# Kernel tuning notes

Hardware: AMD Instinct MI355X
Metric: run time of the kernel (lower is better)

The kernel has to match this reference:

```python
import jax, jax.numpy as jnp
import numpy as np

B, MAXN, D, H, S = 64, 512, 512, 8, 32
DH = D // H          # per-head dim = 64
N = B * MAXN         # 32768 total nodes
E = 524288           # ~avg degree 16
EPS = 1e-5


def setup_inputs() -> dict:
    key = jax.random.key(0)
    ks = jax.random.split(key, 18)
    s = 0.05
    x_dense = jax.random.normal(ks[0], (B, MAXN, D), jnp.float32)
    x = jax.random.normal(ks[1], (N, D), jnp.float32)
    src = jax.random.randint(ks[2], (E,), 0, N)
    # destinations kept within the same graph as the source
    dst = (src // MAXN) * MAXN + jax.random.randint(ks[3], (E,), 0, MAXN)
    edge_index = jnp.stack([src, dst]).astype(jnp.int32)
    batch = (jnp.arange(N) // MAXN).astype(jnp.int32)  # sorted, 512 nodes/graph
    seed = jax.random.normal(ks[4], (S, 1, D), jnp.float32) * s
    # per-head GCN conv weights concatenated along output dim: [D, H*DH] == [D, D]
    Wk = jax.random.normal(ks[5], (D, D), jnp.float32) * s
    bk = jnp.zeros((D,), jnp.float32)
    Wv = jax.random.normal(ks[6], (D, D), jnp.float32) * s
    bv = jnp.zeros((D,), jnp.float32)
    q_proj_weight = jax.random.normal(ks[7], (D, D), jnp.float32) * s
    Wo = jax.random.normal(ks[8], (D, D), jnp.float32) * s
    bo = jnp.zeros((D,), jnp.float32)
    Wff = jax.random.normal(ks[9], (D, D), jnp.float32) * s
    bff = jnp.zeros((D,), jnp.float32)
    gamma_h = jnp.ones((D,), jnp.float32)
    beta_h = jnp.zeros((D,), jnp.float32)
    gamma_z = jnp.ones((D,), jnp.float32)
    beta_z = jnp.zeros((D,), jnp.float32)
    return dict(x_dense=x_dense, x=x, edge_index=edge_index, batch=batch,
                seed=seed, Wk=Wk, bk=bk, Wv=Wv, bv=bv,
                q_proj_weight=q_proj_weight, Wo=Wo, bo=bo, Wff=Wff, bff=bff,
                gamma_h=gamma_h, beta_h=beta_h, gamma_z=gamma_z, beta_z=beta_z)


def _gcn(x, W, b, src, dst):
    # PyG GCNConv with self-loops + symmetric norm; all H heads fused via W [D, H*DH]
    xw = x @ W                                   # [N, D]
    idx = jnp.arange(N)
    src_f = jnp.concatenate([src, idx])
    dst_f = jnp.concatenate([dst, idx])
    deg = jax.ops.segment_sum(jnp.ones_like(dst_f, dtype=x.dtype), dst_f, num_segments=N)
    dinv = jax.lax.rsqrt(deg)                    # deg >= 1 (self-loops)
    norm = dinv[src_f] * dinv[dst_f]             # [E+N]
    out = jax.ops.segment_sum(xw[src_f] * norm[:, None], dst_f, num_segments=N)
    return out + b


def _to_dense(feat, batch):
    # to_dense_batch for sorted batch vector; padded slots are zeros
    counts = jax.ops.segment_sum(jnp.ones((N,), jnp.int32), batch, num_segments=B)
    start = jnp.cumsum(counts) - counts
    pos = jnp.arange(N) - start[batch]
    return jnp.zeros((B, MAXN, feat.shape[-1]), feat.dtype).at[batch, pos].set(feat)


def _layernorm(x, g, b):
    m = jnp.mean(x, -1, keepdims=True)
    v = jnp.mean(jnp.square(x - m), -1, keepdims=True)
    return (x - m) * jax.lax.rsqrt(v + EPS) * g + b


def reference(x_dense, x, edge_index, batch, seed, Wk, bk, Wv, bv,
              q_proj_weight, Wo, bo, Wff, bff, gamma_h, beta_h, gamma_z, beta_z):
    src, dst = edge_index[0], edge_index[1]
    k_nodes = _gcn(x, Wk, bk, src, dst)          # [N, D] (H heads concat)
    v_nodes = _gcn(x, Wv, bv, src, dst)
    k_dense = _to_dense(k_nodes, batch)          # [B, MAXN, D]
    v_dense = _to_dense(v_nodes, batch)

    # query: seed [S,1,D] repeated over batch -> [S,B,D]; q projection (F.linear)
    query = jnp.broadcast_to(seed, (S, B, D))
    q = jnp.einsum('sbd,ed->sbe', query, q_proj_weight)
    scale = 1.0 / jnp.sqrt(jnp.float32(DH))
    qh = (q * scale).reshape(S, B, H, DH).transpose(1, 2, 0, 3)     # [B,H,S,DH]
    kh = k_dense.reshape(B, MAXN, H, DH).transpose(0, 2, 1, 3)      # [B,H,N,DH]
    vh = v_dense.reshape(B, MAXN, H, DH).transpose(0, 2, 1, 3)
    scores = jnp.einsum('bhsd,bhnd->bhsn', qh, kh)                  # [B,H,S,MAXN]
    attn = jax.nn.softmax(scores, axis=-1)                          # no padding mask (faithful)
    ctx = jnp.einsum('bhsn,bhnd->bhsd', attn, vh)                   # [B,H,S,DH]
    ctx = ctx.transpose(0, 2, 1, 3).reshape(B, S, D)                # heads concat
    attn_out = ctx @ Wo.T + bo                                      # [B,S,D]

    query_bse = jnp.broadcast_to(seed.transpose(1, 0, 2), (B, S, D))
    embed = _layernorm(query_bse + attn_out, gamma_h, beta_h)
    embed = _layernorm(embed + embed @ Wff.T + bff, gamma_z, beta_z)
    return embed
```

## Files before the change

kernel.cpp:

```cpp
#include <hip/hip_runtime.h>
#include <hip/hip_bf16.h>

#define BN   64
#define MAXN 512
#define DIM  512
#define NH   8
#define NS   32
#define DHD  64
#define NN   32768
#define NE   524288

typedef __hip_bfloat16 bf16;
using bf16x8 = __attribute__((ext_vector_type(8))) short;
using f32x4  = __attribute__((ext_vector_type(4))) float;

__device__ int   g_cnt[NN];
__device__ int   g_cur[NN];
__device__ int   g_off[NN + 1];
__device__ int   g_csr[NE];
__device__ float g_dinv[NN];
__device__ bf16  g_xb[NN * DIM];
__device__ bf16  g_agg[NN * DIM];
__device__ bf16  g_kv[NN * 2 * DIM];
__device__ bf16  g_wkvT[2 * DIM * DIM];
__device__ bf16  g_woT[DIM * DIM];
__device__ bf16  g_wffT[DIM * DIM];
__device__ float g_biaskv[2 * DIM];
__device__ float g_q[NS * DIM];
__device__ bf16  g_qb[NS * DIM];
__device__ bf16  g_ctx[BN * NS * DIM];
__device__ float g_tmp[BN * NS * DIM];
__device__ float g_h1[BN * NS * DIM];
__device__ bf16  g_h1b[BN * NS * DIM];

__device__ inline float bf2f(unsigned short u) {
    union { unsigned int i; float f; } x; x.i = ((unsigned int)u) << 16; return x.f;
}

__device__ inline void gll16(const bf16* g, bf16* l) {
    __builtin_amdgcn_global_load_lds(
        (const __attribute__((address_space(1))) void*)g,
        (__attribute__((address_space(3))) void*)l, 16, 0, 0);
}

__global__ void k_zero() {
    int i = blockIdx.x * 256 + threadIdx.x;
    if (i < NN) { g_cnt[i] = 0; g_cur[i] = 0; }
}

__global__ void k_count(const int* __restrict__ dst) {
    int e = blockIdx.x * 256 + threadIdx.x;
    if (e < NE) atomicAdd(&g_cnt[dst[e]], 1);
}

__global__ void k_scan() {
    __shared__ int part[1024];
    int t = threadIdx.x;
    int base = t * 32;
    int loc[32]; int s = 0;
#pragma unroll
    for (int i = 0; i < 32; i++) { loc[i] = g_cnt[base + i]; s += loc[i]; }
    part[t] = s; __syncthreads();
    for (int o = 1; o < 1024; o <<= 1) {
        int v = (t >= o) ? part[t - o] : 0;
        __syncthreads();
        part[t] += v;
        __syncthreads();
    }
    int ex = (t == 0) ? 0 : part[t - 1];
#pragma unroll
    for (int i = 0; i < 32; i++) { g_off[base + i] = ex; ex += loc[i]; }
    if (t == 1023) g_off[NN] = ex;
}

__global__ void k_dinv() {
    int i = blockIdx.x * 256 + threadIdx.x;
    if (i < NN) g_dinv[i] = rsqrtf(1.0f + (float)g_cnt[i]);
}

__global__ void k_fill(const int* __restrict__ src, const int* __restrict__ dst) {
    int e = blockIdx.x * 256 + threadIdx.x;
    if (e < NE) {
        int d = dst[e];
        int p = atomicAdd(&g_cur[d], 1);
        g_csr[g_off[d] + p] = src[e];
    }
}

__global__ __launch_bounds__(256) void k_xb(const float* __restrict__ x) {
    long i = (long)(blockIdx.x * 256 + threadIdx.x) * 8;
    int node = (int)(i >> 9);
    float w = g_dinv[node];
    float4 a = *(const float4*)(x + i);
    float4 b = *(const float4*)(x + i + 4);
    float v[8] = {a.x, a.y, a.z, a.w, b.x, b.y, b.z, b.w};
    bf16x8 o;
#pragma unroll
    for (int j = 0; j < 8; j++) { bf16 t = __float2bfloat16(v[j] * w); o[j] = *(short*)&t; }
    *(bf16x8*)(g_xb + i) = o;
}

__global__ __launch_bounds__(256) void k_gather() {
    int bid = blockIdx.x;
    int lb = (bid & 7) * 1024 + (bid >> 3);
    int wave = threadIdx.x >> 6, lane = threadIdx.x & 63;
    int node = lb * 4 + wave;

    bf16x8 sv = ((const bf16x8*)(g_xb + (long)node * DIM))[lane];
    float acc[8];
#pragma unroll
    for (int j = 0; j < 8; j++) acc[j] = bf2f((unsigned short)sv[j]);

    int e = g_off[node], e1 = g_off[node + 1];
    for (; e + 2 <= e1; e += 2) {
        int s0 = g_csr[e], s1 = g_csr[e + 1];
        bf16x8 r0 = ((const bf16x8*)(g_xb + (long)s0 * DIM))[lane];
        bf16x8 r1 = ((const bf16x8*)(g_xb + (long)s1 * DIM))[lane];
#pragma unroll
        for (int j = 0; j < 8; j++)
            acc[j] += bf2f((unsigned short)r0[j]) + bf2f((unsigned short)r1[j]);
    }
    if (e < e1) {
        int s0 = g_csr[e];
        bf16x8 r0 = ((const bf16x8*)(g_xb + (long)s0 * DIM))[lane];
#pragma unroll
        for (int j = 0; j < 8; j++) acc[j] += bf2f((unsigned short)r0[j]);
    }
    float dd = g_dinv[node];
    bf16x8 o;
#pragma unroll
    for (int j = 0; j < 8; j++) { bf16 t = __float2bfloat16(acc[j] * dd); o[j] = *(short*)&t; }
    ((bf16x8*)(g_agg + (long)node * DIM))[lane] = o;
}

__global__ void k_prepw(const float* __restrict__ Wk, const float* __restrict__ Wv,
                        const float* __restrict__ bk, const float* __restrict__ bv,
                        const float* __restrict__ Wo, const float* __restrict__ Wff) {
    int i = blockIdx.x * 256 + threadIdx.x;
    int c = i >> 9, k = i & 511;
    float v = (c < DIM) ? Wk[k * DIM + c] : Wv[k * DIM + (c - DIM)];
    g_wkvT[i] = __float2bfloat16(v);
    if (i < DIM * DIM) {
        g_woT[i]  = __float2bfloat16(Wo[i]);
        g_wffT[i] = __float2bfloat16(Wff[i]);
    }
    if (i < 2 * DIM) g_biaskv[i] = (i < DIM) ? bk[i] : bv[i - DIM];
}

__global__ void k_qproj(const float* __restrict__ seed, const float* __restrict__ Wq) {
    int i = blockIdx.x * 256 + threadIdx.x;
    int s = i >> 9, e = i & 511;
    const float* sr = seed + s * DIM;
    const float* wr = Wq + e * DIM;
    float acc = 0.f;
    for (int d = 0; d < DIM; d += 4) {
        float4 a = *(const float4*)(sr + d);
        float4 b = *(const float4*)(wr + d);
        acc += a.x * b.x + a.y * b.y + a.z * b.z + a.w * b.w;
    }
    float qv = acc * 0.125f;
    g_q[i] = qv;
    g_qb[i] = __float2bfloat16(qv);
}

template<int W>
__global__ __launch_bounds__(256) void k_gemm(const float* __restrict__ biasIn) {
    constexpr int Nout = (W == 0) ? 2 * DIM : DIM;
    const bf16* A  = (W == 0) ? g_agg  : (W == 1) ? g_ctx : g_h1b;
    const bf16* Bt = (W == 0) ? g_wkvT : (W == 1) ? g_woT : g_wffT;
    const float* bias = (W == 0) ? g_biaskv : biasIn;

    __shared__ bf16 As[2][128 * 32];
    __shared__ bf16 Bs[2][128 * 32];
    int tid = threadIdx.x;
    int lane = tid & 63, wave = tid >> 6;
    int wr = wave >> 1, wc = wave & 1;
    long row0 = (long)blockIdx.x * 128, col0 = (long)blockIdx.y * 128;
    f32x4 acc[4][4];
#pragma unroll
    for (int i = 0; i < 4; i++)
#pragma unroll
        for (int j = 0; j < 4; j++) acc[i][j] = (f32x4){0.f, 0.f, 0.f, 0.f};
    int fr = lane & 15, fq = lane >> 4;
    int sw = (fr >> 1) & 3;
    int rchunk = (fq ^ sw) * 8;

    int u0 = wave * 128 + lane;
    int s_row[2], s_col[2];
#pragma unroll
    for (int c = 0; c < 2; c++) {
        int u = u0 + c * 64;
        int row = u >> 2, cc = u & 3;
        s_row[c] = row;
        s_col[c] = (cc ^ ((row >> 1) & 3)) * 8;
    }

    auto stage = [&](int buf, int kt) {
#pragma unroll
        for (int c = 0; c < 2; c++)
            gll16(A + (row0 + s_row[c]) * DIM + kt + s_col[c], As[buf] + (u0 + c * 64) * 8);
#pragma unroll
        for (int c = 0; c < 2; c++)
            gll16(Bt + (col0 + s_row[c]) * DIM + kt + s_col[c], Bs[buf] + (u0 + c * 64) * 8);
    };

    stage(0, 0);
    __syncthreads();

    for (int kt = 0; kt < DIM; kt += 32) {
        int buf = (kt >> 5) & 1;
        if (kt + 32 < DIM) stage(buf ^ 1, kt + 32);
        bf16x8 af[4], bfv[4];
#pragma unroll
        for (int mi = 0; mi < 4; mi++)
            af[mi] = *(const bf16x8*)(As[buf] + (wr * 64 + mi * 16 + fr) * 32 + rchunk);
#pragma unroll
        for (int ni = 0; ni < 4; ni++)
            bfv[ni] = *(const bf16x8*)(Bs[buf] + (wc * 64 + ni * 16 + fr) * 32 + rchunk);
#pragma unroll
        for (int mi = 0; mi < 4; mi++)
#pragma unroll
            for (int ni = 0; ni < 4; ni++)
                acc[mi][ni] = __builtin_amdgcn_mfma_f32_16x16x32_bf16(af[mi], bfv[ni], acc[mi][ni], 0, 0, 0);
        __syncthreads();
    }
#pragma unroll
    for (int mi = 0; mi < 4; mi++)
#pragma unroll
        for (int ni = 0; ni < 4; ni++) {
            long col = col0 + wc * 64 + ni * 16 + fr;
            float bv = bias[col];
#pragma unroll
            for (int r = 0; r < 4; r++) {
                long row = row0 + wr * 64 + mi * 16 + fq * 4 + r;
                float v = acc[mi][ni][r] + bv;
                if constexpr (W == 0) g_kv[row * Nout + col] = __float2bfloat16(v);
                else                  g_tmp[row * Nout + col] = v;
            }
        }
}

__global__ __launch_bounds__(512) void k_attn() {
    __shared__ bf16  kv[64 * 72];
    __shared__ float sc[32 * 516];
    __shared__ float rs[NS];
    int b = blockIdx.x >> 3, h = blockIdx.x & 7;
    int tid = threadIdx.x;
    int lane = tid & 63, w = tid >> 6;
    int fr = lane & 15, fq = lane >> 4;
    int stile = w >> 2;
    int nsub  = w & 3;
    int dht   = w & 3;

    const unsigned short* KV = (const unsigned short*)g_kv + (long)b * MAXN * (2 * DIM) + h * DHD;
    int srow = tid >> 3;
    int scol = (tid & 7) * 8;

    bf16x8 qf[2];
#pragma unroll
    for (int k0 = 0; k0 < 2; k0++)
        qf[k0] = *(const bf16x8*)(g_qb + (long)(stile * 16 + fr) * DIM + h * DHD + k0 * 32 + fq * 8);

    int4 pre = *(const int4*)(KV + (long)srow * (2 * DIM) + scol);
    for (int t = 0; t < 8; t++) {
        __syncthreads();
        *(int4*)((unsigned short*)kv + srow * 72 + scol) = pre;
        if (t < 7) pre = *(const int4*)(KV + (long)((t + 1) * 64 + srow) * (2 * DIM) + scol);
        __syncthreads();
        f32x4 acc = {0.f, 0.f, 0.f, 0.f};
#pragma unroll
        for (int k0 = 0; k0 < 2; k0++) {
            bf16x8 kf = *(const bf16x8*)(kv + (nsub * 16 + fr) * 72 + k0 * 32 + fq * 8);
            acc = __builtin_amdgcn_mfma_f32_16x16x32_bf16(qf[k0], kf, acc, 0, 0, 0);
        }
        int n = t * 64 + nsub * 16 + fr;
#pragma unroll
        for (int r = 0; r < 4; r++)
            sc[(stile * 16 + fq * 4 + r) * 516 + n] = acc[r];
    }
    __syncthreads();

    pre = *(const int4*)(KV + DIM + (long)srow * (2 * DIM) + scol);

#pragma unroll
    for (int r = 0; r < 4; r++) {
        int row = w * 4 + r;
        int base = row * 516 + lane;
        float v[8]; float m = -1e30f;
#pragma unroll
        for (int k = 0; k < 8; k++) { v[k] = sc[base + 64 * k]; m = fmaxf(m, v[k]); }
#pragma unroll
        for (int o = 32; o > 0; o >>= 1) m = fmaxf(m, __shfl_xor(m, o));
        float sum = 0.f;
#pragma unroll
        for (int k = 0; k < 8; k++) { v[k] = __expf(v[k] - m); sum += v[k]; }
#pragma unroll
        for (int o = 32; o > 0; o >>= 1) sum += __shfl_xor(sum, o);
#pragma unroll
        for (int k = 0; k < 8; k++) sc[base + 64 * k] = v[k];
        if (lane == 0) rs[row] = 1.0f / sum;
    }

    f32x4 acc3 = {0.f, 0.f, 0.f, 0.f};
    for (int t = 0; t < 8; t++) {
        __syncthreads();
        *(int4*)((unsigned short*)kv + srow * 72 + scol) = pre;
        if (t < 7) pre = *(const int4*)(KV + DIM + (long)((t + 1) * 64 + srow) * (2 * DIM) + scol);
        __syncthreads();
        const float* Pp = sc + (stile * 16 + fr) * 516 + t * 64;
#pragma unroll
        for (int k0 = 0; k0 < 2; k0++) {
            bf16x8 pa, vb;
#pragma unroll
            for (int i = 0; i < 8; i++) {
                bf16 pb = __float2bfloat16(Pp[k0 * 32 + fq * 8 + i]);
                pa[i] = *(short*)&pb;
                vb[i] = *((const short*)kv + (k0 * 32 + fq * 8 + i) * 72 + dht * 16 + fr);
            }
            acc3 = __builtin_amdgcn_mfma_f32_16x16x32_bf16(pa, vb, acc3, 0, 0, 0);
        }
    }
    int dh = dht * 16 + fr;
    bf16* cp = g_ctx + ((long)(b * NS + stile * 16 + fq * 4)) * DIM + h * DHD + dh;
#pragma unroll
    for (int r = 0; r < 4; r++) {
        int row = stile * 16 + fq * 4 + r;
        cp[(long)r * DIM] = __float2bfloat16(acc3[r] * rs[row]);
    }
}

__device__ inline float blockReduceSum(float v, float* red, int tid) {
#pragma unroll
    for (int o = 32; o > 0; o >>= 1) v += __shfl_xor(v, o);
    __syncthreads();
    if ((tid & 63) == 0) red[tid >> 6] = v;
    __syncthreads();
    return red[0] + red[1] + red[2] + red[3];
}

__global__ __launch_bounds__(256) void k_ln1(const float* __restrict__ seed,
                                             const float* __restrict__ gamma,
                                             const float* __restrict__ beta) {
    __shared__ float red[4];
    int r = blockIdx.x, t = threadIdx.x;
    int s = r & 31;
    long base = (long)r * DIM;
    float v0 = g_tmp[base + t] + seed[s * DIM + t];
    float v1 = g_tmp[base + 256 + t] + seed[s * DIM + 256 + t];
    float mean = blockReduceSum(v0 + v1, red, t) * (1.0f / DIM);
    float d0 = v0 - mean, d1 = v1 - mean;
    float var = blockReduceSum(d0 * d0 + d1 * d1, red, t) * (1.0f / DIM);
    float ri = rsqrtf(var + 1e-5f);
    float o0 = d0 * ri * gamma[t] + beta[t];
    float o1 = d1 * ri * gamma[256 + t] + beta[256 + t];
    g_h1[base + t] = o0; g_h1[base + 256 + t] = o1;
    g_h1b[base + t] = __float2bfloat16(o0);
    g_h1b[base + 256 + t] = __float2bfloat16(o1);
}

__global__ __launch_bounds__(256) void k_ln2(const float* __restrict__ gamma,
                                             const float* __restrict__ beta,
                                             float* __restrict__ out) {
    __shared__ float red[4];
    int r = blockIdx.x, t = threadIdx.x;
    long base = (long)r * DIM;
    float v0 = g_tmp[base + t] + g_h1[base + t];
    float v1 = g_tmp[base + 256 + t] + g_h1[base + 256 + t];
    float mean = blockReduceSum(v0 + v1, red, t) * (1.0f / DIM);
    float d0 = v0 - mean, d1 = v1 - mean;
    float var = blockReduceSum(d0 * d0 + d1 * d1, red, t) * (1.0f / DIM);
    float ri = rsqrtf(var + 1e-5f);
    out[base + t] = d0 * ri * gamma[t] + beta[t];
    out[base + 256 + t] = d1 * ri * gamma[256 + t] + beta[256 + t];
}

extern "C" void kernel_launch(void* const* d_in, const int* in_sizes, int n_in,
                              void* d_out, int out_size, void* d_ws, size_t ws_size,
                              hipStream_t stream) {
    (void)in_sizes; (void)n_in; (void)out_size; (void)d_ws; (void)ws_size;
    const float* x    = (const float*)d_in[1];
    const int*   ei   = (const int*)d_in[2];
    const int*   esrc = ei;
    const int*   edst = ei + NE;
    const float* seed = (const float*)d_in[4];
    const float* Wk   = (const float*)d_in[5];
    const float* bk   = (const float*)d_in[6];
    const float* Wv   = (const float*)d_in[7];
    const float* bv   = (const float*)d_in[8];
    const float* Wq   = (const float*)d_in[9];
    const float* Wo   = (const float*)d_in[10];
    const float* bo   = (const float*)d_in[11];
    const float* Wff  = (const float*)d_in[12];
    const float* bff  = (const float*)d_in[13];
    const float* gh   = (const float*)d_in[14];
    const float* bh   = (const float*)d_in[15];
    const float* gz   = (const float*)d_in[16];
    const float* bz   = (const float*)d_in[17];
    float* out = (float*)d_out;

    k_zero <<<NN / 256, 256, 0, stream>>>();
    k_count<<<NE / 256, 256, 0, stream>>>(edst);
    k_scan <<<1, 1024, 0, stream>>>();
    k_dinv <<<NN / 256, 256, 0, stream>>>();
    k_fill <<<NE / 256, 256, 0, stream>>>(esrc, edst);
    k_xb   <<<(NN * DIM) / (256 * 8), 256, 0, stream>>>(x);
    k_gather<<<NN / 4, 256, 0, stream>>>();
    k_prepw<<<(2 * DIM * DIM) / 256, 256, 0, stream>>>(Wk, Wv, bk, bv, Wo, Wff);
    k_qproj<<<(NS * DIM) / 256, 256, 0, stream>>>(seed, Wq);

    dim3 g1(NN / 128, (2 * DIM) / 128);
    k_gemm<0><<<g1, 256, 0, stream>>>(nullptr);

    k_attn<<<BN * NH, 512, 0, stream>>>();

    dim3 g2((BN * NS) / 128, DIM / 128);
    k_gemm<1><<<g2, 256, 0, stream>>>(bo);
    k_ln1<<<BN * NS, 256, 0, stream>>>(seed, gh, bh);
    k_gemm<2><<<g2, 256, 0, stream>>>(bff);
    k_ln2<<<BN * NS, 256, 0, stream>>>(gz, bz, out);
}
```

Baseline: 239.2 us.

## Fold K/V projections into query and output weights, skip the big KV GEMM

```diff
diff --git a/kernel.cpp b/kernel.cpp
--- a/kernel.cpp
+++ b/kernel.cpp
@@ -21,14 +21,14 @@
 __device__ float g_dinv[NN];
 __device__ bf16  g_xb[NN * DIM];
 __device__ bf16  g_agg[NN * DIM];
-__device__ bf16  g_kv[NN * 2 * DIM];
-__device__ bf16  g_wkvT[2 * DIM * DIM];
-__device__ bf16  g_woT[DIM * DIM];
+__device__ bf16  g_aggT[NN * DIM];
+__device__ bf16  g_qf[256 * DIM];
+__device__ bf16  g_wvo[DIM * 8 * DIM];
+__device__ float g_bvo[DIM];
 __device__ bf16  g_wffT[DIM * DIM];
-__device__ float g_biaskv[2 * DIM];
 __device__ float g_q[NS * DIM];
-__device__ bf16  g_qb[NS * DIM];
-__device__ bf16  g_ctx[BN * NS * DIM];
+__device__ bf16  g_sc[BN * 256 * MAXN];
+__device__ bf16  g_cp[BN * NS * 8 * DIM];
 __device__ float g_tmp[BN * NS * DIM];
 __device__ float g_h1[BN * NS * DIM];
 __device__ bf16  g_h1b[BN * NS * DIM];
@@ -69,13 +69,11 @@
     }
     int ex = (t == 0) ? 0 : part[t - 1];
 #pragma unroll
-    for (int i = 0; i < 32; i++) { g_off[base + i] = ex; ex += loc[i]; }
+    for (int i = 0; i < 32; i++) {
+        g_off[base + i] = ex; ex += loc[i];
+        g_dinv[base + i] = rsqrtf(1.0f + (float)loc[i]);
+    }
     if (t == 1023) g_off[NN] = ex;
-}
-
-__global__ void k_dinv() {
-    int i = blockIdx.x * 256 + threadIdx.x;
-    if (i < NN) g_dinv[i] = rsqrtf(1.0f + (float)g_cnt[i]);
 }
 
 __global__ void k_fill(const int* __restrict__ src, const int* __restrict__ dst) {
@@ -112,15 +110,18 @@
     for (int j = 0; j < 8; j++) acc[j] = bf2f((unsigned short)sv[j]);
 
     int e = g_off[node], e1 = g_off[node + 1];
-    for (; e + 2 <= e1; e += 2) {
-        int s0 = g_csr[e], s1 = g_csr[e + 1];
+    for (; e + 4 <= e1; e += 4) {
+        int s0 = g_csr[e], s1 = g_csr[e + 1], s2 = g_csr[e + 2], s3 = g_csr[e + 3];
         bf16x8 r0 = ((const bf16x8*)(g_xb + (long)s0 * DIM))[lane];
         bf16x8 r1 = ((const bf16x8*)(g_xb + (long)s1 * DIM))[lane];
+        bf16x8 r2 = ((const bf16x8*)(g_xb + (long)s2 * DIM))[lane];
+        bf16x8 r3 = ((const bf16x8*)(g_xb + (long)s3 * DIM))[lane];
 #pragma unroll
         for (int j = 0; j < 8; j++)
-            acc[j] += bf2f((unsigned short)r0[j]) + bf2f((unsigned short)r1[j]);
-    }
-    if (e < e1) {
+            acc[j] += (bf2f((unsigned short)r0[j]) + bf2f((unsigned short)r1[j]))
+                    + (bf2f((unsigned short)r2[j]) + bf2f((unsigned short)r3[j]));
+    }
+    for (; e < e1; e++) {
         int s0 = g_csr[e];
         bf16x8 r0 = ((const bf16x8*)(g_xb + (long)s0 * DIM))[lane];
 #pragma unroll
@@ -133,18 +134,28 @@
     ((bf16x8*)(g_agg + (long)node * DIM))[lane] = o;
 }
 
-__global__ void k_prepw(const float* __restrict__ Wk, const float* __restrict__ Wv,
-                        const float* __restrict__ bk, const float* __restrict__ bv,
-                        const float* __restrict__ Wo, const float* __restrict__ Wff) {
-    int i = blockIdx.x * 256 + threadIdx.x;
-    int c = i >> 9, k = i & 511;
-    float v = (c < DIM) ? Wk[k * DIM + c] : Wv[k * DIM + (c - DIM)];
-    g_wkvT[i] = __float2bfloat16(v);
-    if (i < DIM * DIM) {
-        g_woT[i]  = __float2bfloat16(Wo[i]);
-        g_wffT[i] = __float2bfloat16(Wff[i]);
-    }
-    if (i < 2 * DIM) g_biaskv[i] = (i < DIM) ? bk[i] : bv[i - DIM];
+__global__ __launch_bounds__(256) void k_aggT() {
+    __shared__ unsigned short L[64][72];
+    int id = blockIdx.x;
+    int b = id >> 6, t = id & 63;
+    int n0 = (t & 7) * 64, d0 = (t >> 3) * 64;
+    int tid = threadIdx.x;
+    const unsigned short* src = (const unsigned short*)g_agg + ((long)b * 512 + n0) * 512 + d0;
+#pragma unroll
+    for (int p = 0; p < 2; p++) {
+        int r = (tid >> 3) + 32 * p, c = (tid & 7) * 8;
+        *(int4*)&L[r][c] = *(const int4*)(src + (long)r * 512 + c);
+    }
+    __syncthreads();
+    unsigned short* dst = (unsigned short*)g_aggT + ((long)b * 512 + d0) * 512 + n0;
+#pragma unroll
+    for (int p = 0; p < 2; p++) {
+        int dr = (tid >> 3) + 32 * p, c0 = (tid & 7) * 8;
+        unsigned short tmp[8];
+#pragma unroll
+        for (int j = 0; j < 8; j++) tmp[j] = L[c0 + j][dr];
+        *(int4*)(dst + (long)dr * 512 + c0) = *(int4*)tmp;
+    }
 }
 
 __global__ void k_qproj(const float* __restrict__ seed, const float* __restrict__ Wq) {
@@ -158,17 +169,57 @@
         float4 b = *(const float4*)(wr + d);
         acc += a.x * b.x + a.y * b.y + a.z * b.z + a.w * b.w;
     }
-    float qv = acc * 0.125f;
-    g_q[i] = qv;
-    g_qb[i] = __float2bfloat16(qv);
-}
-
-template<int W>
-__global__ __launch_bounds__(256) void k_gemm(const float* __restrict__ biasIn) {
-    constexpr int Nout = (W == 0) ? 2 * DIM : DIM;
-    const bf16* A  = (W == 0) ? g_agg  : (W == 1) ? g_ctx : g_h1b;
-    const bf16* Bt = (W == 0) ? g_wkvT : (W == 1) ? g_woT : g_wffT;
-    const float* bias = (W == 0) ? g_biaskv : biasIn;
+    g_q[i] = acc * 0.125f;
+}
+
+__global__ __launch_bounds__(256) void k_fold(const float* __restrict__ Wk,
+                                              const float* __restrict__ Wv,
+                                              const float* __restrict__ Wo,
+                                              const float* __restrict__ bo,
+                                              const float* __restrict__ bv,
+                                              const float* __restrict__ Wff) {
+    int blk = blockIdx.x;
+    if (blk < 512) {
+        int i = blk * 256 + threadIdx.x;
+        int hs = i >> 9, d = i & 511;
+        int h = hs >> 5, s = hs & 31;
+        const float* qr = g_q + s * DIM + h * 64;
+        const float* wr = Wk + d * DIM + h * 64;
+        float acc = 0.f;
+        for (int t2 = 0; t2 < 64; t2 += 4) {
+            float4 a = *(const float4*)(qr + t2);
+            float4 w = *(const float4*)(wr + t2);
+            acc += a.x * w.x + a.y * w.y + a.z * w.z + a.w * w.w;
+        }
+        g_qf[i] = __float2bfloat16(acc);
+    } else if (blk < 8704) {
+        int j = (blk - 512) * 256 + threadIdx.x;
+        int e = j >> 12, hd = j & 4095, h = hd >> 9, d = hd & 511;
+        const float* vr = Wv + d * DIM + h * 64;
+        const float* orow = Wo + e * DIM + h * 64;
+        float acc = 0.f;
+        for (int t2 = 0; t2 < 64; t2 += 4) {
+            float4 a = *(const float4*)(vr + t2);
+            float4 w = *(const float4*)(orow + t2);
+            acc += a.x * w.x + a.y * w.y + a.z * w.z + a.w * w.w;
+        }
+        g_wvo[j] = __float2bfloat16(acc);
+    } else if (blk < 8706) {
+        int e = (blk - 8704) * 256 + threadIdx.x;
+        float acc = bo[e];
+        const float* orow = Wo + e * DIM;
+        for (int c = 0; c < DIM; c++) acc += bv[c] * orow[c];
+        g_bvo[e] = acc;
+    } else {
+        int i = (blk - 8706) * 256 + threadIdx.x;
+        g_wffT[i] = __float2bfloat16(Wff[i]);
+    }
+}
+
+__global__ __launch_bounds__(256) void k_scores() {
+    const bf16* A  = g_qf;
+    const bf16* Bt = g_agg + (long)blockIdx.z * (MAXN * DIM);
+    bf16* out = g_sc + (long)blockIdx.z * (256 * MAXN);
 
     __shared__ bf16 As[2][128 * 32];
     __shared__ bf16 Bs[2][128 * 32];
@@ -182,8 +233,7 @@
 #pragma unroll
         for (int j = 0; j < 4; j++) acc[i][j] = (f32x4){0.f, 0.f, 0.f, 0.f};
     int fr = lane & 15, fq = lane >> 4;
-    int sw = (fr >> 1) & 3;
-    int rchunk = (fq ^ sw) * 8;
+    int rchunk = (fq ^ ((fr >> 1) & 3)) * 8;
 
     int u0 = wave * 128 + lane;
     int s_row[2], s_col[2];
@@ -229,66 +279,44 @@
 #pragma unroll
         for (int ni = 0; ni < 4; ni++) {
             long col = col0 + wc * 64 + ni * 16 + fr;
-            float bv = bias[col];
 #pragma unroll
             for (int r = 0; r < 4; r++) {
                 long row = row0 + wr * 64 + mi * 16 + fq * 4 + r;
-                float v = acc[mi][ni][r] + bv;
-                if constexpr (W == 0) g_kv[row * Nout + col] = __float2bfloat16(v);
-                else                  g_tmp[row * Nout + col] = v;
+                out[row * MAXN + col] = __float2bfloat16(acc[mi][ni][r]);
             }
         }
 }
 
-__global__ __launch_bounds__(512) void k_attn() {
-    __shared__ bf16  kv[64 * 72];
-    __shared__ float sc[32 * 516];
-    __shared__ float rs[NS];
-    int b = blockIdx.x >> 3, h = blockIdx.x & 7;
-    int tid = threadIdx.x;
-    int lane = tid & 63, w = tid >> 6;
+__global__ __launch_bounds__(256) void k_pv() {
+    __shared__ bf16 Pl[32 * 512];
+    __shared__ bf16 Bs[2][256 * 32];
+    int id = blockIdx.x;
+    int b = id >> 4, h = (id >> 1) & 7, dh = id & 1;
+    int tid = threadIdx.x, lane = tid & 63, w = tid >> 6;
     int fr = lane & 15, fq = lane >> 4;
-    int stile = w >> 2;
-    int nsub  = w & 3;
-    int dht   = w & 3;
-
-    const unsigned short* KV = (const unsigned short*)g_kv + (long)b * MAXN * (2 * DIM) + h * DHD;
-    int srow = tid >> 3;
-    int scol = (tid & 7) * 8;
-
-    bf16x8 qf[2];
-#pragma unroll
-    for (int k0 = 0; k0 < 2; k0++)
-        qf[k0] = *(const bf16x8*)(g_qb + (long)(stile * 16 + fr) * DIM + h * DHD + k0 * 32 + fq * 8);
-
-    int4 pre = *(const int4*)(KV + (long)srow * (2 * DIM) + scol);
-    for (int t = 0; t < 8; t++) {
-        __syncthreads();
-        *(int4*)((unsigned short*)kv + srow * 72 + scol) = pre;
-        if (t < 7) pre = *(const int4*)(KV + (long)((t + 1) * 64 + srow) * (2 * DIM) + scol);
-        __syncthreads();
-        f32x4 acc = {0.f, 0.f, 0.f, 0.f};
-#pragma unroll
-        for (int k0 = 0; k0 < 2; k0++) {
-            bf16x8 kf = *(const bf16x8*)(kv + (nsub * 16 + fr) * 72 + k0 * 32 + fq * 8);
-            acc = __builtin_amdgcn_mfma_f32_16x16x32_bf16(qf[k0], kf, acc, 0, 0, 0);
-        }
-        int n = t * 64 + nsub * 16 + fr;
-#pragma unroll
-        for (int r = 0; r < 4; r++)
-            sc[(stile * 16 + fq * 4 + r) * 516 + n] = acc[r];
-    }
-    __syncthreads();
-
-    pre = *(const int4*)(KV + DIM + (long)srow * (2 * DIM) + scol);
-
-#pragma unroll
-    for (int r = 0; r < 4; r++) {
-        int row = w * 4 + r;
-        int base = row * 516 + lane;
+
+    const bf16* BT = g_aggT + (long)b * (DIM * MAXN) + (long)dh * (256 * MAXN);
+    int srow[4], scol[4];
+#pragma unroll
+    for (int c = 0; c < 4; c++) {
+        int u = tid + 256 * c;
+        srow[c] = u >> 2;
+        scol[c] = ((u & 3) ^ ((srow[c] >> 1) & 3)) * 8;
+    }
+    auto stage = [&](int buf, int kt) {
+#pragma unroll
+        for (int c = 0; c < 4; c++)
+            gll16(BT + (long)srow[c] * MAXN + kt + scol[c], Bs[buf] + (tid + 256 * c) * 8);
+    };
+    stage(0, 0);
+
+    const unsigned short* scp = (const unsigned short*)g_sc + ((long)b * 256 + (long)h * 32) * MAXN;
+#pragma unroll
+    for (int r = 0; r < 8; r++) {
+        int row = w * 8 + r;
         float v[8]; float m = -1e30f;
 #pragma unroll
-        for (int k = 0; k < 8; k++) { v[k] = sc[base + 64 * k]; m = fmaxf(m, v[k]); }
+        for (int k = 0; k < 8; k++) { v[k] = bf2f(scp[row * MAXN + lane + 64 * k]); m = fmaxf(m, v[k]); }
 #pragma unroll
         for (int o = 32; o > 0; o >>= 1) m = fmaxf(m, __shfl_xor(m, o));
         float sum = 0.f;
@@ -296,37 +324,121 @@
         for (int k = 0; k < 8; k++) { v[k] = __expf(v[k] - m); sum += v[k]; }
 #pragma unroll
         for (int o = 32; o > 0; o >>= 1) sum += __shfl_xor(sum, o);
-#pragma unroll
-        for (int k = 0; k < 8; k++) sc[base + 64 * k] = v[k];
-        if (lane == 0) rs[row] = 1.0f / sum;
-    }
-
-    f32x4 acc3 = {0.f, 0.f, 0.f, 0.f};
-    for (int t = 0; t < 8; t++) {
+        float inv = 1.0f / sum;
+#pragma unroll
+        for (int k = 0; k < 8; k++) {
+            int col = lane + 64 * k;
+            int chunk = (col >> 3) ^ (row & 7);
+            Pl[row * 512 + chunk * 8 + (col & 7)] = __float2bfloat16(v[k] * inv);
+        }
+    }
+    __syncthreads();
+
+    f32x4 acc[2][4];
+#pragma unroll
+    for (int i = 0; i < 2; i++)
+#pragma unroll
+        for (int j = 0; j < 4; j++) acc[i][j] = (f32x4){0.f, 0.f, 0.f, 0.f};
+
+    for (int kt = 0; kt < MAXN; kt += 32) {
+        int buf = (kt >> 5) & 1;
+        if (kt + 32 < MAXN) stage(buf ^ 1, kt + 32);
+        bf16x8 pa[2], vb[4];
+#pragma unroll
+        for (int mi = 0; mi < 2; mi++) {
+            int pr = mi * 16 + fr;
+            int slot = ((kt >> 3) + fq) ^ (pr & 7);
+            pa[mi] = *(const bf16x8*)(Pl + pr * 512 + slot * 8);
+        }
+#pragma unroll
+        for (int nf = 0; nf < 4; nf++) {
+            int dr = w * 64 + nf * 16 + fr;
+            vb[nf] = *(const bf16x8*)(Bs[buf] + dr * 32 + (fq ^ ((dr >> 1) & 3)) * 8);
+        }
+#pragma unroll
+        for (int mi = 0; mi < 2; mi++)
+#pragma unroll
+            for (int nf = 0; nf < 4; nf++)
+                acc[mi][nf] = __builtin_amdgcn_mfma_f32_16x16x32_bf16(pa[mi], vb[nf], acc[mi][nf], 0, 0, 0);
         __syncthreads();
-        *(int4*)((unsigned short*)kv + srow * 72 + scol) = pre;
-        if (t < 7) pre = *(const int4*)(KV + DIM + (long)((t + 1) * 64 + srow) * (2 * DIM) + scol);
+    }
+#pragma unroll
+    for (int mi = 0; mi < 2; mi++)
+#pragma unroll
+        for (int nf = 0; nf < 4; nf++) {
+            int d = w * 64 + nf * 16 + fr;
+#pragma unroll
+            for (int r = 0; r < 4; r++) {
+                int s = mi * 16 + fq * 4 + r;
+                g_cp[((long)b * NS + s) * 4096 + h * 512 + dh * 256 + d] =
+                    __float2bfloat16(acc[mi][nf][r]);
+            }
+        }
+}
+
+template<int KD, bool FFN>
+__global__ __launch_bounds__(256) void k_gemm64(const float* __restrict__ biasIn) {
+    const bf16* A  = FFN ? g_h1b : g_cp;
+    const bf16* Bt = FFN ? g_wffT : g_wvo;
+
+    __shared__ bf16 As[2][64 * 32];
+    __shared__ bf16 Bs[2][64 * 32];
+    int tid = threadIdx.x;
+    int lane = tid & 63, wave = tid >> 6;
+    int wr = wave >> 1, wc = wave & 1;
+    long row0 = (long)blockIdx.x * 64, col0 = (long)blockIdx.y * 64;
+    f32x4 acc[2][2];
+#pragma unroll
+    for (int i = 0; i < 2; i++)
+#pragma unroll
+        for (int j = 0; j < 2; j++) acc[i][j] = (f32x4){0.f, 0.f, 0.f, 0.f};
+    int fr = lane & 15, fq = lane >> 4;
+
+    int srow = tid >> 2, scc = tid & 3;
+    int scol = (scc ^ ((srow >> 1) & 3)) * 8;
+
+    auto stage = [&](int buf, int kt) {
+        gll16(A  + (row0 + srow) * KD + kt + scol, As[buf] + tid * 8);
+        gll16(Bt + (col0 + srow) * KD + kt + scol, Bs[buf] + tid * 8);
+    };
+
+    stage(0, 0);
+    __syncthreads();
+
+    for (int kt = 0; kt < KD; kt += 32) {
+        int buf = (kt >> 5) & 1;
+        if (kt + 32 < KD) stage(buf ^ 1, kt + 32);
+        bf16x8 af[2], bfv[2];
+#pragma unroll
+        for (int mi = 0; mi < 2; mi++) {
+            int ar = wr * 32 + mi * 16 + fr;
+            af[mi] = *(const bf16x8*)(As[buf] + ar * 32 + (fq ^ ((ar >> 1) & 3)) * 8);
+        }
+#pragma unroll
+        for (int ni = 0; ni < 2; ni++) {
+            int br = wc * 32 + ni * 16 + fr;
+            bfv[ni] = *(const bf16x8*)(Bs[buf] + br * 32 + (fq ^ ((br >> 1) & 3)) * 8);
+        }
+#pragma unroll
+        for (int mi = 0; mi < 2; mi++)
+#pragma unroll
+            for (int ni = 0; ni < 2; ni++)
+                acc[mi][ni] = __builtin_amdgcn_mfma_f32_16x16x32_bf16(af[mi], bfv[ni], acc[mi][ni], 0, 0, 0);
         __syncthreads();
-        const float* Pp = sc + (stile * 16 + fr) * 516 + t * 64;
-#pragma unroll
-        for (int k0 = 0; k0 < 2; k0++) {
-            bf16x8 pa, vb;
-#pragma unroll
-            for (int i = 0; i < 8; i++) {
-                bf16 pb = __float2bfloat16(Pp[k0 * 32 + fq * 8 + i]);
-                pa[i] = *(short*)&pb;
-                vb[i] = *((const short*)kv + (k0 * 32 + fq * 8 + i) * 72 + dht * 16 + fr);
+    }
+    const float* bias = FFN ? biasIn : g_bvo;
+#pragma unroll
+    for (int mi = 0; mi < 2; mi++)
+#pragma unroll
+        for (int ni = 0; ni < 2; ni++) {
+            long col = col0 + wc * 32 + ni * 16 + fr;
+            float bv = bias[col];
+#pragma unroll
+            for (int r = 0; r < 4; r++) {
+                long row = row0 + wr * 32 + mi * 16 + fq * 4 + r;
+                g_tmp[row * DIM + col] = acc[mi][ni][r] + bv;
             }
-            acc3 = __builtin_amdgcn_mfma_f32_16x16x32_bf16(pa, vb, acc3, 0, 0, 0);
-        }
-    }
-    int dh = dht * 16 + fr;
-    bf16* cp = g_ctx + ((long)(b * NS + stile * 16 + fq * 4)) * DIM + h * DHD + dh;
-#pragma unroll
-    for (int r = 0; r < 4; r++) {
-        int row = stile * 16 + fq * 4 + r;
-        cp[(long)r * DIM] = __float2bfloat16(acc3[r] * rs[row]);
-    }
+        }
 }
 
 __device__ inline float blockReduceSum(float v, float* red, int tid) {
@@ -384,7 +496,6 @@
     const int*   edst = ei + NE;
     const float* seed = (const float*)d_in[4];
     const float* Wk   = (const float*)d_in[5];
-    const float* bk   = (const float*)d_in[6];
     const float* Wv   = (const float*)d_in[7];
     const float* bv   = (const float*)d_in[8];
     const float* Wq   = (const float*)d_in[9];
@@ -401,21 +512,21 @@
     k_zero <<<NN / 256, 256, 0, stream>>>();
     k_count<<<NE / 256, 256, 0, stream>>>(edst);
     k_scan <<<1, 1024, 0, stream>>>();
-    k_dinv <<<NN / 256, 256, 0, stream>>>();
     k_fill <<<NE / 256, 256, 0, stream>>>(esrc, edst);
     k_xb   <<<(NN * DIM) / (256 * 8), 256, 0, stream>>>(x);
     k_gather<<<NN / 4, 256, 0, stream>>>();
-    k_prepw<<<(2 * DIM * DIM) / 256, 256, 0, stream>>>(Wk, Wv, bk, bv, Wo, Wff);
+    k_aggT <<<BN * 64, 256, 0, stream>>>();
     k_qproj<<<(NS * DIM) / 256, 256, 0, stream>>>(seed, Wq);
-
-    dim3 g1(NN / 128, (2 * DIM) / 128);
-    k_gemm<0><<<g1, 256, 0, stream>>>(nullptr);
-
-    k_attn<<<BN * NH, 512, 0, stream>>>();
-
-    dim3 g2((BN * NS) / 128, DIM / 128);
-    k_gemm<1><<<g2, 256, 0, stream>>>(bo);
+    k_fold <<<9730, 256, 0, stream>>>(Wk, Wv, Wo, bo, bv, Wff);
+
+    dim3 gs(2, 4, BN);
+    k_scores<<<gs, 256, 0, stream>>>();
+
+    k_pv<<<BN * 16, 256, 0, stream>>>();
+
+    dim3 g64(32, 8);
+    k_gemm64<4096, false><<<g64, 256, 0, stream>>>(nullptr);
     k_ln1<<<BN * NS, 256, 0, stream>>>(seed, gh, bh);
-    k_gemm<2><<<g2, 256, 0, stream>>>(bff);
+    k_gemm64<512, true><<<g64, 256, 0, stream>>>(bff);
     k_ln2<<<BN * NS, 256, 0, stream>>>(gz, bz, out);
 }
```

Result: slower. 374.9 us (+56.7%).
